# Optimization experiments

Measured on AMD Instinct MI355X. Metric: run time of the kernel, lower is better.

The kernel has to match this reference:

```python
import jax, jax.numpy as jnp
import numpy as np

DIM = 1024
N_EXPERTS = 8
TOP_K = 2
B, S = 2, 1024


def setup_inputs() -> dict:
    key = jax.random.key(0)
    ks = jax.random.split(key, 4)
    scale = 0.02
    return {
        "u_t": jax.random.normal(ks[0], (B, S, DIM), dtype=jnp.float32),
        "centroids": jax.random.normal(ks[1], (N_EXPERTS, DIM), dtype=jnp.float32),
        "score_biases": jnp.zeros((N_EXPERTS,), dtype=jnp.float32),
        "W1": jax.random.normal(ks[2], (N_EXPERTS, DIM, 4 * DIM), dtype=jnp.float32) * scale,
        "b1": jnp.zeros((N_EXPERTS, 4 * DIM), dtype=jnp.float32),
        "W2": jax.random.normal(ks[3], (N_EXPERTS, 4 * DIM, DIM), dtype=jnp.float32) * scale,
        "b2": jnp.zeros((N_EXPERTS, DIM), dtype=jnp.float32),
    }


def reference(u_t, centroids, score_biases, W1, b1, W2, b2):
    Bs, Ss, dim = u_t.shape
    T = Bs * Ss
    N = centroids.shape[0]
    K = TOP_K

    u_flat = u_t.reshape(T, dim)
    scores = u_flat @ centroids.T + score_biases          # [T, N]
    gate = jax.nn.softmax(scores, axis=-1)                # [T, N]
    topk_vals, topk_idx = jax.lax.top_k(gate, K)          # [T, K]

    flat_idx = topk_idx.reshape(-1)                       # [T*K]

    # load-violation stats (no grad path; pure counts)
    perfect_load = K * T / N
    f_i = jnp.zeros((N,), dtype=jnp.float32).at[flat_idx].add(1.0)
    maxvio = (jnp.max(f_i) - perfect_load) / perfect_load

    # Grouped MLP expressed as dense per-expert compute over all tokens,
    # then combined with a sparse [T, N] gate matrix (same math as masked dispatch).
    h = jax.nn.relu(jnp.einsum("td,ndh->nth", u_flat, W1) + b1[:, None, :])  # [N, T, 4*dim]
    expert_outs = jnp.einsum("nth,nhd->ntd", h, W2) + b2[:, None, :]          # [N, T, dim]

    rows = jnp.repeat(jnp.arange(T), K)
    combine_w = jnp.zeros((T, N), dtype=topk_vals.dtype).at[rows, flat_idx].add(topk_vals.reshape(-1))
    out = jnp.einsum("tn,ntd->td", combine_w, expert_outs).reshape(Bs, Ss, dim)
    return (out, maxvio)
```

## Files before the change

### kernel.cpp

```cpp
#include <hip/hip_runtime.h>
#include <hip/hip_bf16.h>

#define T_TOK 2048
#define DIMS  1024
#define HID   4096
#define NE    8
#define BM 128
#define BN 128
#define BK 64

typedef __bf16 bf16x8 __attribute__((ext_vector_type(8)));
typedef float  f32x4  __attribute__((ext_vector_type(4)));

__device__ __forceinline__ unsigned short f2bf(float f) {
  unsigned u = __float_as_uint(f);
  u += 0x7FFFu + ((u >> 16) & 1u);
  return (unsigned short)(u >> 16);
}
__device__ __forceinline__ float bf2f(unsigned short s) {
  return __uint_as_float(((unsigned)s) << 16);
}

__device__ __forceinline__ void g2l16(const void* g, void* l) {
  __builtin_amdgcn_global_load_lds((const __attribute__((address_space(1))) void*)g,
                                   (__attribute__((address_space(3))) void*)l,
                                   16, 0, 0);
}

__device__ __forceinline__ void transcode_tile(const float* __restrict__ src,
    unsigned short* __restrict__ dst, int src_ld, int dst_ld, int r0, int c0,
    unsigned short* lds, int tid) {
  int rbase = tid >> 5;
  int c4l = (tid & 31) * 4;
#pragma unroll 4
  for (int it = 0; it < 16; it++) {
    int r = rbase + it * 8;
    float4 v = *(const float4*)(src + (size_t)(r0 + r) * src_ld + c0 + c4l);
    unsigned short b[4];
    b[0] = f2bf(v.x); b[1] = f2bf(v.y); b[2] = f2bf(v.z); b[3] = f2bf(v.w);
#pragma unroll
    for (int j = 0; j < 4; j++) {
      int c = c4l + j;
      int chunk = it ^ ((c >> 2) & 15);
      lds[c * 128 + chunk * 8 + rbase] = b[j];
    }
  }
  __syncthreads();
  int ck = tid & 15;
  int cb = tid >> 4;
#pragma unroll 4
  for (int it = 0; it < 8; it++) {
    int c = cb + it * 16;
    int chunk = ck ^ ((c >> 2) & 15);
    uint4 v = *(const uint4*)(&lds[c * 128 + chunk * 8]);
    *(uint4*)(dst + (size_t)(c0 + c) * dst_ld + r0 + ck * 8) = v;
  }
}

__global__ __launch_bounds__(256) void k_route(const float* __restrict__ u,
    const float* __restrict__ cent, const float* __restrict__ sbias,
    int* __restrict__ topk_idx, float* __restrict__ topk_val,
    unsigned short* __restrict__ ub,
    const float* __restrict__ W1, unsigned short* __restrict__ w1t) {
  __shared__ __align__(16) unsigned short tlds[128 * 128];
  if (blockIdx.x >= 512) {
    int rank = (int)blockIdx.x - 512;
    int te = rank >> 8, tt = rank & 255;
    int r0 = (tt & 7) * 128, c0 = (tt >> 3) * 128;
    transcode_tile(W1 + (size_t)te * DIMS * HID, w1t + (size_t)te * HID * DIMS,
                   HID, DIMS, r0, c0, tlds, threadIdx.x);
    return;
  }
  int wave = threadIdx.x >> 6;
  int lane = threadIdx.x & 63;
  int t = blockIdx.x * 4 + wave;
  const float* ur = u + (size_t)t * DIMS;
  float p[NE];
#pragma unroll
  for (int n = 0; n < NE; n++) p[n] = 0.f;
#pragma unroll
  for (int ch = 0; ch < 4; ch++) {
    int d = ch * 256 + lane * 4;
    float4 uv = *(const float4*)(ur + d);
    ushort4 o4;
    o4.x = f2bf(uv.x); o4.y = f2bf(uv.y); o4.z = f2bf(uv.z); o4.w = f2bf(uv.w);
    *(ushort4*)(ub + (size_t)t * DIMS + d) = o4;
#pragma unroll
    for (int n = 0; n < NE; n++) {
      float4 cv = *(const float4*)(cent + n * DIMS + d);
      p[n] += uv.x * cv.x + uv.y * cv.y + uv.z * cv.z + uv.w * cv.w;
    }
  }
#pragma unroll
  for (int n = 0; n < NE; n++) {
#pragma unroll
    for (int o = 32; o > 0; o >>= 1) p[n] += __shfl_xor(p[n], o);
  }
  if (lane == 0) {
    float g[NE];
    float m = -1e30f;
#pragma unroll
    for (int n = 0; n < NE; n++) { g[n] = p[n] + sbias[n]; m = fmaxf(m, g[n]); }
    float sum = 0.f;
#pragma unroll
    for (int n = 0; n < NE; n++) { g[n] = expf(g[n] - m); sum += g[n]; }
    float inv = 1.f / sum;
#pragma unroll
    for (int n = 0; n < NE; n++) g[n] *= inv;
    int i0 = 0;
#pragma unroll
    for (int n = 1; n < NE; n++) if (g[n] > g[i0]) i0 = n;
    int i1 = (i0 == 0) ? 1 : 0;
#pragma unroll
    for (int n = 0; n < NE; n++) if (n != i0 && g[n] > g[i1]) i1 = n;
    topk_idx[2 * t] = i0;     topk_idx[2 * t + 1] = i1;
    topk_val[2 * t] = g[i0];  topk_val[2 * t + 1] = g[i1];
  }
}

__global__ __launch_bounds__(256) void k_finalize(const int* __restrict__ topk_idx,
    int* __restrict__ cnt, int* __restrict__ offs, float* __restrict__ maxvio,
    int* __restrict__ rowtok, int* __restrict__ pairpos) {
  __shared__ int sc[256][NE];
  __shared__ int sof[NE];
  int tid = threadIdx.x;
  int el[16];
  int c[NE];
#pragma unroll
  for (int n = 0; n < NE; n++) c[n] = 0;
#pragma unroll
  for (int i = 0; i < 16; i++) {
    el[i] = topk_idx[tid * 16 + i];
#pragma unroll
    for (int n = 0; n < NE; n++) c[n] += (el[i] == n) ? 1 : 0;
  }
#pragma unroll
  for (int n = 0; n < NE; n++) sc[tid][n] = c[n];
  __syncthreads();
  for (int st = 1; st < 256; st <<= 1) {
    int v[NE];
#pragma unroll
    for (int n = 0; n < NE; n++) v[n] = (tid >= st) ? sc[tid - st][n] : 0;
    __syncthreads();
#pragma unroll
    for (int n = 0; n < NE; n++) sc[tid][n] += v[n];
    __syncthreads();
  }
  if (tid == 0) {
    int o = 0, mx = 0;
#pragma unroll
    for (int n = 0; n < NE; n++) {
      int t = sc[255][n];
      cnt[n] = t; offs[n] = o; sof[n] = o;
      o += t; mx = max(mx, t);
    }
    maxvio[0] = ((float)mx - 512.f) / 512.f;
  }
  __syncthreads();
  int base[NE];
#pragma unroll
  for (int n = 0; n < NE; n++) base[n] = sof[n] + sc[tid][n] - c[n];
#pragma unroll
  for (int i = 0; i < 16; i++) {
    int eN = el[i];
    int pos = 0;
#pragma unroll
    for (int n = 0; n < NE; n++) if (eN == n) { pos = base[n]; base[n] = pos + 1; }
    rowtok[pos] = (tid * 16 + i) >> 1;
    pairpos[tid * 16 + i] = pos;
  }
}

__global__ __launch_bounds__(256) void k_gemm1n(const unsigned short* __restrict__ ub,
    const unsigned short* __restrict__ w1t, const float* __restrict__ b1,
    const int* __restrict__ rowtok, const int* __restrict__ cnts, const int* __restrict__ offs,
    unsigned short* __restrict__ h,
    const float* __restrict__ W2, unsigned short* __restrict__ w2t) {
  __shared__ __align__(16) unsigned char smem[65536];
  int tid = threadIdx.x;
  int e = blockIdx.z;
  int cnt = cnts[e];
  int m0 = blockIdx.y * BM;

  if (m0 >= cnt) {
    int live[NE];
#pragma unroll
    for (int z = 0; z < NE; z++) live[z] = min(16, (cnts[z] + BM - 1) >> 7);
    int rank = 0;
    for (int z = 0; z < e; z++) rank += (16 - live[z]) * 32;
    rank += ((int)blockIdx.y - live[e]) * 32 + (int)blockIdx.x;
    if (rank >= 2048) return;
    int te = rank >> 8, tt = rank & 255;
    transcode_tile(W2 + (size_t)te * HID * DIMS, w2t + (size_t)te * HID * DIMS,
                   DIMS, HID, (tt & 31) * 128, (tt >> 5) * 128,
                   (unsigned short*)smem, tid);
    return;
  }

  int off = offs[e];
  int n0 = blockIdx.x * BN;
  int lane = tid & 63;
  int wm = (tid >> 7) & 1;
  int wn = (tid >> 6) & 1;
  int srow = tid >> 3;
  int cp = tid & 7;
  const unsigned short* gA[4];
  const unsigned short* gB[4];
#pragma unroll
  for (int a = 0; a < 4; a++) {
    int r = a * 32 + srow;
    int c = cp ^ (r & 7);
    int pr = min(off + m0 + r, off + cnt - 1);
    int tok = rowtok[pr];
    gA[a] = ub + (size_t)tok * DIMS + c * 8;
    gB[a] = w1t + ((size_t)e * HID + (n0 + r)) * DIMS + c * 8;
  }
  unsigned wboff = (unsigned)__builtin_amdgcn_readfirstlane((tid >> 6) << 10);
  f32x4 acc[4][4];
  f32x4 zz = {0.f, 0.f, 0.f, 0.f};
#pragma unroll
  for (int i = 0; i < 4; i++)
#pragma unroll
    for (int j = 0; j < 4; j++) acc[i][j] = zz;

  int lane15 = lane & 15, quad = lane >> 4, l7 = lane & 7;
  unsigned aOff = (unsigned)((wm * 64 + lane15) * 128);
  unsigned bOff = (unsigned)(16384 + (wn * 64 + lane15) * 128);

#pragma unroll
  for (int a = 0; a < 4; a++) g2l16(gA[a], smem + a * 4096 + wboff);
#pragma unroll
  for (int a = 0; a < 4; a++) g2l16(gB[a], smem + 16384 + a * 4096 + wboff);

#pragma unroll 1
  for (int it = 0; it < DIMS / BK; it++) {
    unsigned base = (unsigned)((it & 1) << 15);
    unsigned nb = base ^ 32768u;
    if (it + 1 < DIMS / BK) {
      int k1 = (it + 1) * BK;
#pragma unroll
      for (int a = 0; a < 4; a++) g2l16(gA[a] + k1, smem + nb + a * 4096 + wboff);
#pragma unroll
      for (int a = 0; a < 4; a++) g2l16(gB[a] + k1, smem + nb + 16384 + a * 4096 + wboff);
      asm volatile("s_waitcnt vmcnt(8)" ::: "memory");
    } else {
      asm volatile("s_waitcnt vmcnt(0)" ::: "memory");
    }
    __builtin_amdgcn_s_barrier();
    __builtin_amdgcn_sched_barrier(0);
#pragma unroll
    for (int s = 0; s < 2; s++) {
      unsigned cpf = (unsigned)(((s * 4 + quad) ^ l7) * 16);
      bf16x8 af[4], bfr[4];
#pragma unroll
      for (int i = 0; i < 4; i++) af[i] = *(const bf16x8*)(smem + base + aOff + i * 2048 + cpf);
#pragma unroll
      for (int j = 0; j < 4; j++) bfr[j] = *(const bf16x8*)(smem + base + bOff + j * 2048 + cpf);
#pragma unroll
      for (int i = 0; i < 4; i++)
#pragma unroll
        for (int j = 0; j < 4; j++)
          acc[i][j] = __builtin_amdgcn_mfma_f32_16x16x32_bf16(af[i], bfr[j], acc[i][j], 0, 0, 0);
    }
    __builtin_amdgcn_sched_barrier(0);
    asm volatile("s_waitcnt lgkmcnt(0)" ::: "memory");
    __builtin_amdgcn_s_barrier();
  }
  float b1v[4];
#pragma unroll
  for (int j = 0; j < 4; j++) b1v[j] = b1[e * HID + n0 + wn * 64 + j * 16 + lane15];
#pragma unroll
  for (int i = 0; i < 4; i++) {
#pragma unroll
    for (int r = 0; r < 4; r++) {
      int mrow = m0 + wm * 64 + i * 16 + quad * 4 + r;
      if (mrow < cnt) {
        size_t hrow = (size_t)(off + mrow) * HID;
#pragma unroll
        for (int j = 0; j < 4; j++) {
          int col = n0 + wn * 64 + j * 16 + lane15;
          float v = fmaxf(acc[i][j][r] + b1v[j], 0.f);
          h[hrow + col] = f2bf(v);
        }
      }
    }
  }
}

__global__ __launch_bounds__(256) void k_gemm1o(const unsigned short* __restrict__ ub,
    const float* __restrict__ W1, const float* __restrict__ b1,
    const int* __restrict__ rowtok, const int* __restrict__ cnts, const int* __restrict__ offs,
    unsigned short* __restrict__ h,
    const float* __restrict__ W2, unsigned short* __restrict__ w2t) {
  __shared__ __align__(16) unsigned char smem[32768];
  int tid = threadIdx.x;
  int e = blockIdx.z;
  int cnt = cnts[e];
  int m0 = blockIdx.y * BM;

  if (m0 >= cnt) {
    int live[NE];
#pragma unroll
    for (int z = 0; z < NE; z++) live[z] = min(16, (cnts[z] + BM - 1) >> 7);
    int rank = 0;
    for (int z = 0; z < e; z++) rank += (16 - live[z]) * 32;
    rank += ((int)blockIdx.y - live[e]) * 32 + (int)blockIdx.x;
    if (rank >= 2048) return;
    int te = rank >> 8, tt = rank & 255;
    transcode_tile(W2 + (size_t)te * HID * DIMS, w2t + (size_t)te * HID * DIMS,
                   DIMS, HID, (tt & 31) * 128, (tt >> 5) * 128,
                   (unsigned short*)smem, tid);
    return;
  }

  int off = offs[e];
  int n0 = blockIdx.x * BN;
  int lane = tid & 63;
  int wv = tid >> 6;
  int wm = (tid >> 7) & 1;
  int wn = (tid >> 6) & 1;
  int srow = tid >> 3;
  int cp = tid & 7;
  const float* w1e = W1 + (size_t)e * DIMS * HID;
  const unsigned short* gAp[4];
#pragma unroll
  for (int a = 0; a < 4; a++) {
    int r = a * 32 + srow;
    int c = cp ^ (r & 7);
    int pr = min(off + m0 + r, off + cnt - 1);
    int tok = rowtok[pr];
    gAp[a] = ub + (size_t)tok * DIMS + c * 8;
  }
  int wboff = __builtin_amdgcn_readfirstlane(wv << 10);
  f32x4 acc[4][4];
  f32x4 zz = {0.f, 0.f, 0.f, 0.f};
#pragma unroll
  for (int i = 0; i < 4; i++)
#pragma unroll
    for (int j = 0; j < 4; j++) acc[i][j] = zz;

  int lane15 = lane & 15, quad = lane >> 4, l7 = lane & 7;
  unsigned aRowOff = (unsigned)((wm * 64 + lane15) * 128);
  unsigned bRowOff = (unsigned)(16384 + (wn * 64 + lane15) * 128);

#pragma unroll 1
  for (int k0 = 0; k0 < DIMS; k0 += BK) {
#pragma unroll
    for (int a = 0; a < 4; a++) g2l16(gAp[a] + k0, smem + a * 4096 + wboff);
#pragma unroll
    for (int jj = 0; jj < 4; jj++) {
      int j = wv * 4 + jj;
      int kc = j & 7, nh = j >> 3;
      int nloc = nh * 64 + lane;
      const float* src = w1e + (size_t)(k0 + kc * 8) * HID + n0 + nloc;
      float t0, t1, t2, t3, t4, t5, t6, t7;
      t0 = src[0];            t1 = src[(size_t)HID];
      t2 = src[(size_t)2 * HID]; t3 = src[(size_t)3 * HID];
      t4 = src[(size_t)4 * HID]; t5 = src[(size_t)5 * HID];
      t6 = src[(size_t)6 * HID]; t7 = src[(size_t)7 * HID];
      bf16x8 pk;
      pk[0] = (__bf16)t0; pk[1] = (__bf16)t1; pk[2] = (__bf16)t2; pk[3] = (__bf16)t3;
      pk[4] = (__bf16)t4; pk[5] = (__bf16)t5; pk[6] = (__bf16)t6; pk[7] = (__bf16)t7;
      int cs = kc ^ (lane & 7);
      *(bf16x8*)(smem + 16384 + nloc * 128 + cs * 16) = pk;
    }
    __syncthreads();
#pragma unroll
    for (int s = 0; s < 2; s++) {
      unsigned cpf = (unsigned)(((s * 4 + quad) ^ l7) * 16);
      bf16x8 af[4], bfr[4];
#pragma unroll
      for (int i = 0; i < 4; i++) af[i] = *(const bf16x8*)(smem + aRowOff + i * 2048 + cpf);
#pragma unroll
      for (int j = 0; j < 4; j++) bfr[j] = *(const bf16x8*)(smem + bRowOff + j * 2048 + cpf);
#pragma unroll
      for (int i = 0; i < 4; i++)
#pragma unroll
        for (int j = 0; j < 4; j++)
          acc[i][j] = __builtin_amdgcn_mfma_f32_16x16x32_bf16(af[i], bfr[j], acc[i][j], 0, 0, 0);
    }
    __syncthreads();
  }
  float b1v[4];
#pragma unroll
  for (int j = 0; j < 4; j++) b1v[j] = b1[e * HID + n0 + wn * 64 + j * 16 + lane15];
#pragma unroll
  for (int i = 0; i < 4; i++) {
#pragma unroll
    for (int r = 0; r < 4; r++) {
      int mrow = m0 + wm * 64 + i * 16 + quad * 4 + r;
      if (mrow < cnt) {
        size_t hrow = (size_t)(off + mrow) * HID;
#pragma unroll
        for (int j = 0; j < 4; j++) {
          int col = n0 + wn * 64 + j * 16 + lane15;
          float v = fmaxf(acc[i][j][r] + b1v[j], 0.f);
          h[hrow + col] = f2bf(v);
        }
      }
    }
  }
}

__global__ __launch_bounds__(256) void k_gemm2(const unsigned short* __restrict__ hbuf,
    const unsigned short* __restrict__ w2t, const float* __restrict__ b2,
    const int* __restrict__ cnts, const int* __restrict__ offs,
    unsigned short* __restrict__ pout, int KC) {
  int z = blockIdx.z;
  int e = z & 7;
  int sp = z >> 3;
  int cnt = cnts[e];
  int m0 = blockIdx.y * BM;
  if (m0 >= cnt) return;
  int off = offs[e];
  int n0 = blockIdx.x * BN;
  __shared__ __align__(16) unsigned char smem[65536];

  int tid = threadIdx.x;
  int lane = tid & 63;
  int wm = (tid >> 7) & 1;
  int wn = (tid >> 6) & 1;
  int srow = tid >> 3;
  int cp = tid & 7;
  const unsigned short* gA[4];
  const unsigned short* gB[4];
#pragma unroll
  for (int a = 0; a < 4; a++) {
    int r = a * 32 + srow;
    int c = cp ^ (r & 7);
    int pr = min(off + m0 + r, off + cnt - 1);
    gA[a] = hbuf + (size_t)pr * HID + c * 8;
    gB[a] = w2t + ((size_t)e * DIMS + (n0 + r)) * HID + c * 8;
  }
  unsigned wboff = (unsigned)__builtin_amdgcn_readfirstlane((tid >> 6) << 10);
  f32x4 acc[4][4];
  f32x4 zz = {0.f, 0.f, 0.f, 0.f};
#pragma unroll
  for (int i = 0; i < 4; i++)
#pragma unroll
    for (int j = 0; j < 4; j++) acc[i][j] = zz;

  int lane15 = lane & 15, quad = lane >> 4, l7 = lane & 7;
  unsigned aOff = (unsigned)((wm * 64 + lane15) * 128);
  unsigned bOff = (unsigned)(16384 + (wn * 64 + lane15) * 128);

  int kbeg = sp * KC;
  int NIT = KC / BK;
#pragma unroll
  for (int a = 0; a < 4; a++) g2l16(gA[a] + kbeg, smem + a * 4096 + wboff);
#pragma unroll
  for (int a = 0; a < 4; a++) g2l16(gB[a] + kbeg, smem + 16384 + a * 4096 + wboff);

#pragma unroll 1
  for (int it = 0; it < NIT; it++) {
    unsigned base = (unsigned)((it & 1) << 15);
    unsigned nb = base ^ 32768u;
    if (it + 1 < NIT) {
      int k1 = kbeg + (it + 1) * BK;
#pragma unroll
      for (int a = 0; a < 4; a++) g2l16(gA[a] + k1, smem + nb + a * 4096 + wboff);
#pragma unroll
      for (int a = 0; a < 4; a++) g2l16(gB[a] + k1, smem + nb + 16384 + a * 4096 + wboff);
      asm volatile("s_waitcnt vmcnt(8)" ::: "memory");
    } else {
      asm volatile("s_waitcnt vmcnt(0)" ::: "memory");
    }
    __builtin_amdgcn_s_barrier();
    __builtin_amdgcn_sched_barrier(0);
#pragma unroll
    for (int s = 0; s < 2; s++) {
      unsigned cpf = (unsigned)(((s * 4 + quad) ^ l7) * 16);
      bf16x8 af[4], bfr[4];
#pragma unroll
      for (int i = 0; i < 4; i++) af[i] = *(const bf16x8*)(smem + base + aOff + i * 2048 + cpf);
#pragma unroll
      for (int j = 0; j < 4; j++) bfr[j] = *(const bf16x8*)(smem + base + bOff + j * 2048 + cpf);
#pragma unroll
      for (int i = 0; i < 4; i++)
#pragma unroll
        for (int j = 0; j < 4; j++)
          acc[i][j] = __builtin_amdgcn_mfma_f32_16x16x32_bf16(af[i], bfr[j], acc[i][j], 0, 0, 0);
    }
    __builtin_amdgcn_sched_barrier(0);
    asm volatile("s_waitcnt lgkmcnt(0)" ::: "memory");
    __builtin_amdgcn_s_barrier();
  }
  float b2v[4];
#pragma unroll
  for (int j = 0; j < 4; j++)
    b2v[j] = (sp == 0) ? b2[e * DIMS + n0 + wn * 64 + j * 16 + lane15] : 0.f;
  unsigned short* pme = pout + (size_t)sp * T_TOK * 2 * DIMS;
#pragma unroll
  for (int i = 0; i < 4; i++) {
#pragma unroll
    for (int r = 0; r < 4; r++) {
      int mrow = m0 + wm * 64 + i * 16 + quad * 4 + r;
      if (mrow < cnt) {
        size_t prow = (size_t)(off + mrow) * DIMS;
#pragma unroll
        for (int j = 0; j < 4; j++) {
          int col = n0 + wn * 64 + j * 16 + lane15;
          pme[prow + col] = f2bf(acc[i][j][r] + b2v[j]);
        }
      }
    }
  }
}

__global__ __launch_bounds__(256) void k_combine(const unsigned short* __restrict__ pout,
    const int* __restrict__ pairpos, const float* __restrict__ tkv,
    float* __restrict__ out, int nsplit) {
  int t = blockIdx.x;
  int d = threadIdx.x * 4;
  int p0 = pairpos[2 * t], p1 = pairpos[2 * t + 1];
  float w0 = tkv[2 * t], w1 = tkv[2 * t + 1];
  float a0 = 0.f, a1 = 0.f, a2 = 0.f, a3 = 0.f;
  float c0 = 0.f, c1 = 0.f, c2 = 0.f, c3 = 0.f;
  const size_t SS = (size_t)T_TOK * 2 * DIMS;
  for (int s = 0; s < nsplit; s++) {
    ushort4 av = *(const ushort4*)(pout + s * SS + (size_t)p0 * DIMS + d);
    ushort4 bv = *(const ushort4*)(pout + s * SS + (size_t)p1 * DIMS + d);
    a0 += bf2f(av.x); a1 += bf2f(av.y); a2 += bf2f(av.z); a3 += bf2f(av.w);
    c0 += bf2f(bv.x); c1 += bf2f(bv.y); c2 += bf2f(bv.z); c3 += bf2f(bv.w);
  }
  float4 o;
  o.x = w0 * a0 + w1 * c0;
  o.y = w0 * a1 + w1 * c1;
  o.z = w0 * a2 + w1 * c2;
  o.w = w0 * a3 + w1 * c3;
  *(float4*)(out + (size_t)t * DIMS + d) = o;
}

extern "C" void kernel_launch(void* const* d_in, const int* in_sizes, int n_in,
                              void* d_out, int out_size, void* d_ws, size_t ws_size,
                              hipStream_t stream) {
  const float* u     = (const float*)d_in[0];
  const float* cent  = (const float*)d_in[1];
  const float* sbias = (const float*)d_in[2];
  const float* W1    = (const float*)d_in[3];
  const float* b1    = (const float*)d_in[4];
  const float* W2    = (const float*)d_in[5];
  const float* b2    = (const float*)d_in[6];
  float* out = (float*)d_out;

  char* ws = (char*)d_ws;
  unsigned short* ubuf = (unsigned short*)(ws);
  unsigned short* hbuf = (unsigned short*)(ws + 4194304);
  unsigned short* w2t  = (unsigned short*)(ws + 37748736);
  const size_t REG4 = 104857600ull;
  const size_t PSZ = (size_t)T_TOK * 2 * DIMS * 2;
  const size_t NEED_NEW = REG4 + 67108864ull + 1048576ull;

  if (ws_size >= NEED_NEW) {
    unsigned short* w1t   = (unsigned short*)(ws + REG4);
    unsigned short* poutb = (unsigned short*)(ws + REG4);
    const int nsplit = 2;
    char* r = ws + REG4 + 67108864ull;
    int*   cnt      = (int*)(r);
    int*   offs     = (int*)(r + 64);
    int*   topk_idx = (int*)(r + 256);
    float* topk_val = (float*)(r + 256 + 16384);
    int*   rowtok   = (int*)(r + 256 + 32768);
    int*   pairpos  = (int*)(r + 256 + 49152);

    k_route<<<2560, 256, 0, stream>>>(u, cent, sbias, topk_idx, topk_val, ubuf, W1, w1t);
    k_finalize<<<1, 256, 0, stream>>>(topk_idx, cnt, offs, out + 2097152, rowtok, pairpos);
    k_gemm1n<<<dim3(32, 16, 8), 256, 0, stream>>>(ubuf, w1t, b1, rowtok, cnt, offs, hbuf,
                                                  W2, w2t);
    k_gemm2<<<dim3(8, 16, 8 * nsplit), 256, 0, stream>>>(hbuf, w2t, b2, cnt, offs,
                                                         poutb, HID / nsplit);
    k_combine<<<2048, 256, 0, stream>>>(poutb, pairpos, topk_val, out, nsplit);
  } else {
    int nsplit = (ws_size >= REG4 + 4 * PSZ + (1u << 20)) ? 4 : 1;
    unsigned short* poutb = (unsigned short*)(ws + REG4);
    char* r = ws + REG4 + (size_t)nsplit * PSZ;
    int*   cnt      = (int*)(r);
    int*   offs     = (int*)(r + 64);
    int*   topk_idx = (int*)(r + 256);
    float* topk_val = (float*)(r + 256 + 16384);
    int*   rowtok   = (int*)(r + 256 + 32768);
    int*   pairpos  = (int*)(r + 256 + 49152);

    k_route<<<512, 256, 0, stream>>>(u, cent, sbias, topk_idx, topk_val, ubuf, W1, ubuf);
    k_finalize<<<1, 256, 0, stream>>>(topk_idx, cnt, offs, out + 2097152, rowtok, pairpos);
    k_gemm1o<<<dim3(32, 16, 8), 256, 0, stream>>>(ubuf, W1, b1, rowtok, cnt, offs, hbuf,
                                                  W2, w2t);
    k_gemm2<<<dim3(8, 16, 8 * nsplit), 256, 0, stream>>>(hbuf, w2t, b2, cnt, offs,
                                                         poutb, HID / nsplit);
    k_combine<<<2048, 256, 0, stream>>>(poutb, pairpos, topk_val, out, nsplit);
  }
}
```

Baseline: 435.0 us.

## Fold routing finalize into route kernel via last-block counter; raise gemm2 split-K to 4

The separate single-block k_finalize launch is removed. Each routing block now increments a global counter, and the last of the 512 routing blocks computes expert counts, offsets, maxvio, rowtok and pairpos, reusing the transpose LDS buffer for the prefix scan. A memset of the counter is added before the route kernel, so one kernel launch is traded for a memset plus atomic and fence overhead. Separately, gemm2's K-split in the large-workspace path goes from 2 to 4. That adds parallelism to gemm2 but doubles the partial-output traffic that k_combine must read.

```diff
diff --git a/kernel.cpp b/kernel.cpp
--- a/kernel.cpp
+++ b/kernel.cpp
@@ -61,18 +61,23 @@
     const float* __restrict__ cent, const float* __restrict__ sbias,
     int* __restrict__ topk_idx, float* __restrict__ topk_val,
     unsigned short* __restrict__ ub,
-    const float* __restrict__ W1, unsigned short* __restrict__ w1t) {
+    const float* __restrict__ W1, unsigned short* __restrict__ w1t,
+    int* __restrict__ done,
+    int* __restrict__ cnt, int* __restrict__ offs, float* __restrict__ maxvio,
+    int* __restrict__ rowtok, int* __restrict__ pairpos) {
   __shared__ __align__(16) unsigned short tlds[128 * 128];
+  __shared__ int amLastS;
+  int tid = threadIdx.x;
   if (blockIdx.x >= 512) {
     int rank = (int)blockIdx.x - 512;
     int te = rank >> 8, tt = rank & 255;
     int r0 = (tt & 7) * 128, c0 = (tt >> 3) * 128;
     transcode_tile(W1 + (size_t)te * DIMS * HID, w1t + (size_t)te * HID * DIMS,
-                   HID, DIMS, r0, c0, tlds, threadIdx.x);
+                   HID, DIMS, r0, c0, tlds, tid);
     return;
   }
-  int wave = threadIdx.x >> 6;
-  int lane = threadIdx.x & 63;
+  int wave = tid >> 6;
+  int lane = tid & 63;
   int t = blockIdx.x * 4 + wave;
   const float* ur = u + (size_t)t * DIMS;
   float p[NE];
@@ -115,6 +120,59 @@
     for (int n = 0; n < NE; n++) if (n != i0 && g[n] > g[i1]) i1 = n;
     topk_idx[2 * t] = i0;     topk_idx[2 * t + 1] = i1;
     topk_val[2 * t] = g[i0];  topk_val[2 * t + 1] = g[i1];
+  }
+  __syncthreads();
+  __threadfence();
+  if (tid == 0) amLastS = (atomicAdd(done, 1) == 511) ? 1 : 0;
+  __syncthreads();
+  if (!amLastS) return;
+  __threadfence();
+  int* sc = (int*)tlds;
+  __shared__ int sof[NE];
+  int el[16];
+  int c[NE];
+#pragma unroll
+  for (int n = 0; n < NE; n++) c[n] = 0;
+#pragma unroll
+  for (int i = 0; i < 16; i++) {
+    el[i] = topk_idx[tid * 16 + i];
+#pragma unroll
+    for (int n = 0; n < NE; n++) c[n] += (el[i] == n) ? 1 : 0;
+  }
+#pragma unroll
+  for (int n = 0; n < NE; n++) sc[tid * NE + n] = c[n];
+  __syncthreads();
+  for (int st = 1; st < 256; st <<= 1) {
+    int v[NE];
+#pragma unroll
+    for (int n = 0; n < NE; n++) v[n] = (tid >= st) ? sc[(tid - st) * NE + n] : 0;
+    __syncthreads();
+#pragma unroll
+    for (int n = 0; n < NE; n++) sc[tid * NE + n] += v[n];
+    __syncthreads();
+  }
+  if (tid == 0) {
+    int o = 0, mx = 0;
+#pragma unroll
+    for (int n = 0; n < NE; n++) {
+      int tt = sc[255 * NE + n];
+      cnt[n] = tt; offs[n] = o; sof[n] = o;
+      o += tt; mx = max(mx, tt);
+    }
+    maxvio[0] = ((float)mx - 512.f) / 512.f;
+  }
+  __syncthreads();
+  int base[NE];
+#pragma unroll
+  for (int n = 0; n < NE; n++) base[n] = sof[n] + sc[tid * NE + n] - c[n];
+#pragma unroll
+  for (int i = 0; i < 16; i++) {
+    int eN = el[i];
+    int pos = 0;
+#pragma unroll
+    for (int n = 0; n < NE; n++) if (eN == n) { pos = base[n]; base[n] = pos + 1; }
+    rowtok[pos] = (tid * 16 + i) >> 1;
+    pairpos[tid * 16 + i] = pos;
   }
 }
 
@@ -554,7 +612,7 @@
   if (ws_size >= NEED_NEW) {
     unsigned short* w1t   = (unsigned short*)(ws + REG4);
     unsigned short* poutb = (unsigned short*)(ws + REG4);
-    const int nsplit = 2;
+    const int nsplit = 4;
     char* r = ws + REG4 + 67108864ull;
     int*   cnt      = (int*)(r);
     int*   offs     = (int*)(r + 64);
@@ -562,9 +620,12 @@
     float* topk_val = (float*)(r + 256 + 16384);
     int*   rowtok   = (int*)(r + 256 + 32768);
     int*   pairpos  = (int*)(r + 256 + 49152);
-
-    k_route<<<2560, 256, 0, stream>>>(u, cent, sbias, topk_idx, topk_val, ubuf, W1, w1t);
-    k_finalize<<<1, 256, 0, stream>>>(topk_idx, cnt, offs, out + 2097152, rowtok, pairpos);
+    int*   done     = (int*)(r + 256 + 65536);
+
+    hipMemsetAsync(done, 0, 4, stream);
+    k_route<<<2560, 256, 0, stream>>>(u, cent, sbias, topk_idx, topk_val, ubuf,
+                                      W1, w1t, done,
+                                      cnt, offs, out + 2097152, rowtok, pairpos);
     k_gemm1n<<<dim3(32, 16, 8), 256, 0, stream>>>(ubuf, w1t, b1, rowtok, cnt, offs, hbuf,
                                                   W2, w2t);
     k_gemm2<<<dim3(8, 16, 8 * nsplit), 256, 0, stream>>>(hbuf, w2t, b2, cnt, offs,
@@ -580,9 +641,12 @@
     float* topk_val = (float*)(r + 256 + 16384);
     int*   rowtok   = (int*)(r + 256 + 32768);
     int*   pairpos  = (int*)(r + 256 + 49152);
-
-    k_route<<<512, 256, 0, stream>>>(u, cent, sbias, topk_idx, topk_val, ubuf, W1, ubuf);
-    k_finalize<<<1, 256, 0, stream>>>(topk_idx, cnt, offs, out + 2097152, rowtok, pairpos);
+    int*   done     = (int*)(r + 256 + 65536);
+
+    hipMemsetAsync(done, 0, 4, stream);
+    k_route<<<512, 256, 0, stream>>>(u, cent, sbias, topk_idx, topk_val, ubuf,
+                                     W1, ubuf, done,
+                                     cnt, offs, out + 2097152, rowtok, pairpos);
     k_gemm1o<<<dim3(32, 16, 8), 256, 0, stream>>>(ubuf, W1, b1, rowtok, cnt, offs, hbuf,
                                                   W2, w2t);
     k_gemm2<<<dim3(8, 16, 8 * nsplit), 256, 0, stream>>>(hbuf, w2t, b2, cnt, offs,
```

After: 497.7 us. 1.14x slower.
